# Optimization experiments

Measured on AMD Instinct MI355X. Metric: run time of the kernel, lower is better.

The kernel has to match this reference:

```python
import jax, jax.numpy as jnp
import numpy as np

N_T, D_MODEL, RANK, BATCH = 64, 1024, 8, 4096
THRESHOLD = 0.0  # jumprelu threshold (forward default)


def setup_inputs() -> dict:
    key = jax.random.key(0)
    k_x, k_v, k_u, k_e = jax.random.split(key, 4)
    scale = (1.0 / (D_MODEL * RANK)) ** 0.25
    x = jax.random.normal(k_x, (BATCH, D_MODEL), dtype=jnp.float32)
    V = jax.random.normal(k_v, (N_T, RANK, D_MODEL), dtype=jnp.float32) * scale
    U = jax.random.normal(k_u, (N_T, D_MODEL, RANK), dtype=jnp.float32) * scale
    encoder = jax.random.normal(k_e, (N_T, D_MODEL), dtype=jnp.float32)
    encoder = encoder / jnp.linalg.norm(encoder, axis=1, keepdims=True)
    bias = -jnp.ones((N_T,), dtype=jnp.float32)  # init_constant(bias, -1.0)
    return {"x": x, "V": V, "U": U, "encoder": encoder, "bias": bias}


def jumprelu(x, threshold=THRESHOLD):
    # forward: hard threshold x * 1[x > threshold]
    return x * (x > threshold).astype(x.dtype)


def reference(x, V, U, encoder, bias):
    # pre_acts: (batch, n)
    pre_acts = x @ encoder.T - bias
    gate = jumprelu(pre_acts)  # activation_fn='jumprelu', threshold=0.0
    # Vx: (n, batch, rank)
    Vx = jnp.einsum('nrd,bd->nbr', V, x)
    # UVx: (n, batch, d) -- the large intermediate a fused kernel would avoid
    UVx = jnp.einsum('ndr,nbr->nbd', U, Vx)
    # gated sum over transforms: (batch, d)
    output = jnp.einsum('nbd,bn->bd', UVx, gate)
    u_norms = jnp.linalg.norm(U.reshape(U.shape[0], -1), axis=1)
    v_norms = jnp.linalg.norm(V.reshape(V.shape[0], -1), axis=1)
    frobenius_norms = u_norms * v_norms / (D_MODEL * RANK) ** 0.5
    return output, gate, frobenius_norms
```

## Files before the change

kernel.cpp:

```cpp
#include <hip/hip_runtime.h>
#include <math.h>

#define BATCHN 4096
#define DMODEL 1024
#define NT 64
#define RANK 8
#define K2 512

typedef __attribute__((ext_vector_type(8))) short bf16x8;
typedef __attribute__((ext_vector_type(4))) float f32x4;

__device__ __forceinline__ void async16(void* lds, const void* g) {
    __builtin_amdgcn_global_load_lds(
        (const __attribute__((address_space(1))) void*)g,
        (__attribute__((address_space(3))) void*)lds, 16, 0, 0);
}

__device__ __forceinline__ short f2bf(float f) {
    unsigned u = __builtin_bit_cast(unsigned, f);
    u += 0x7fffu + ((u >> 16) & 1u);
    return (short)(u >> 16);
}

__device__ __forceinline__ bf16x8 cvt8(const float4 a, const float4 b) {
    bf16x8 o;
    o[0]=f2bf(a.x); o[1]=f2bf(a.y); o[2]=f2bf(a.z); o[3]=f2bf(a.w);
    o[4]=f2bf(b.x); o[5]=f2bf(b.y); o[6]=f2bf(b.z); o[7]=f2bf(b.w);
    return o;
}

__global__ __launch_bounds__(256) void gatevx_kernel(
    const float* __restrict__ x, const float* __restrict__ enc,
    const float* __restrict__ V, const float* __restrict__ U,
    const float* __restrict__ bias,
    float* __restrict__ gate_out, unsigned short* __restrict__ vx_out,
    unsigned short* __restrict__ Ub,
    float* __restrict__ su_part, float* __restrict__ sv_part)
{
    __shared__ unsigned short As[2][4096];
    __shared__ unsigned short Bs[2][4096];
    __shared__ float red[4];
    const int t = threadIdx.x;
    const int bn = blockIdx.x, bm = blockIdx.y;
    const int wave = t >> 6, lane = t & 63;

    if (bn == 9) {
        const int n = bm;
        const size_t base = (size_t)n * 8192;
        float s = 0.f;
        #pragma unroll
        for (int it = 0; it < 4; ++it) {
            const size_t e = base + it * 2048 + t * 8;
            float4 v0 = *(const float4*)(U + e);
            float4 v1 = *(const float4*)(U + e + 4);
            *(bf16x8*)(Ub + e) = cvt8(v0, v1);
            s += v0.x*v0.x + v0.y*v0.y + v0.z*v0.z + v0.w*v0.w
               + v1.x*v1.x + v1.y*v1.y + v1.z*v1.z + v1.w*v1.w;
        }
        #pragma unroll
        for (int off = 32; off; off >>= 1) s += __shfl_down(s, off);
        if ((t & 63) == 0) red[t >> 6] = s;
        __syncthreads();
        if (t == 0) su_part[n] = red[0] + red[1] + red[2] + red[3];
        return;
    }

    constexpr int BK = 64, KDIM = DMODEL, NIT = KDIM / BK;
    const int wm = wave & 1, wn = wave >> 1;
    const int lrow = lane >> 3, lchunk = lane & 7;
    const int l15 = lane & 15, lq = lane >> 4;

    f32x4 acc[2][2] = {};
    const size_t Arow0 = (size_t)bm * 64;
    const float* Bbase = (bn == 0) ? enc : V + (size_t)(bn - 1) * 64 * DMODEL;
    const bool doSV = (bn >= 1) && (bm == 0);
    float sv[2] = {0.f, 0.f};

    auto LOADAB = [&](int k0, float4* a, float4* b) {
        #pragma unroll
        for (int c = 0; c < 2; ++c) {
            const int row = (wave * 2 + c) * 8 + lrow;
            const int chunk = lchunk ^ lrow;
            const float* ax = x + (Arow0 + row) * DMODEL + k0 + chunk * 8;
            a[c*2]   = *(const float4*)ax;
            a[c*2+1] = *(const float4*)(ax + 4);
            const float* bx = Bbase + (size_t)row * DMODEL + k0 + chunk * 8;
            b[c*2]   = *(const float4*)bx;
            b[c*2+1] = *(const float4*)(bx + 4);
        }
    };
    auto WRITEAB = [&](int buf, const float4* a, const float4* b) {
        #pragma unroll
        for (int c = 0; c < 2; ++c) {
            *(bf16x8*)&As[buf][(wave * 2 + c) * 512 + lane * 8] = cvt8(a[c*2], a[c*2+1]);
            *(bf16x8*)&Bs[buf][(wave * 2 + c) * 512 + lane * 8] = cvt8(b[c*2], b[c*2+1]);
            if (doSV) {
                const float4 b0 = b[c*2], b1 = b[c*2+1];
                sv[c] += b0.x*b0.x + b0.y*b0.y + b0.z*b0.z + b0.w*b0.w
                       + b1.x*b1.x + b1.y*b1.y + b1.z*b1.z + b1.w*b1.w;
            }
        }
    };
    auto COMPUTE = [&](int buf) {
        #pragma unroll
        for (int s = 0; s < 2; ++s) {
            bf16x8 af[2], bfr[2];
            const int kc = s * 4 + lq;
            #pragma unroll
            for (int i = 0; i < 2; ++i) {
                const int m = wm * 32 + i * 16 + l15;
                af[i] = *(const bf16x8*)&As[buf][m * BK + ((kc ^ (m & 7)) * 8)];
            }
            #pragma unroll
            for (int j = 0; j < 2; ++j) {
                const int n = wn * 32 + j * 16 + l15;
                bfr[j] = *(const bf16x8*)&Bs[buf][n * BK + ((kc ^ (n & 7)) * 8)];
            }
            #pragma unroll
            for (int i = 0; i < 2; ++i)
                #pragma unroll
                for (int j = 0; j < 2; ++j)
                    acc[i][j] = __builtin_amdgcn_mfma_f32_16x16x32_bf16(
                        af[i], bfr[j], acc[i][j], 0, 0, 0);
        }
    };

    {
        float4 a[4], b[4];
        LOADAB(0, a, b);
        WRITEAB(0, a, b);
    }
    __syncthreads();
    int cur = 0;
    for (int kt = 0; kt < NIT - 1; ++kt) {
        float4 a[4], b[4];
        LOADAB((kt + 1) * BK, a, b);
        COMPUTE(cur);
        WRITEAB(cur ^ 1, a, b);
        __syncthreads();
        cur ^= 1;
    }
    COMPUTE(cur);

    if (doSV) {
        #pragma unroll
        for (int c = 0; c < 2; ++c) {
            float s = sv[c];
            #pragma unroll
            for (int off = 32; off; off >>= 1) s += __shfl_down(s, off);
            if (lane == 0) sv_part[(bn - 1) * 8 + wave * 2 + c] = s;
        }
    }
    __syncthreads();

    if (bn == 0) {
        float* Cs = (float*)&As[0][0];
        #pragma unroll
        for (int i = 0; i < 2; ++i) {
            const int rowb = wm * 32 + i * 16 + lq * 4;
            #pragma unroll
            for (int j = 0; j < 2; ++j) {
                const int col = wn * 32 + j * 16 + l15;
                const float bz = bias[col];
                #pragma unroll
                for (int r = 0; r < 4; ++r) {
                    const float p = acc[i][j][r] - bz;
                    Cs[(rowb + r) * 64 + col] = p > 0.f ? p : 0.f;
                }
            }
        }
        __syncthreads();
        #pragma unroll
        for (int p = 0; p < 4; ++p) {
            const int row = p * 16 + (t >> 4);
            const int col = (t & 15) * 4;
            *(f32x4*)&gate_out[(size_t)(bm * 64 + row) * NT + col] =
                *(const f32x4*)&Cs[row * 64 + col];
        }
    } else {
        unsigned short* Cs16 = &As[0][0];
        #pragma unroll
        for (int i = 0; i < 2; ++i) {
            const int rowb = wm * 32 + i * 16 + lq * 4;
            #pragma unroll
            for (int j = 0; j < 2; ++j) {
                const int col = wn * 32 + j * 16 + l15;
                #pragma unroll
                for (int r = 0; r < 4; ++r)
                    Cs16[(rowb + r) * 64 + col] = (unsigned short)f2bf(acc[i][j][r]);
            }
        }
        __syncthreads();
        #pragma unroll
        for (int p = 0; p < 2; ++p) {
            const int row = p * 32 + (t >> 3);
            const int chunk = t & 7;
            *(bf16x8*)&vx_out[(size_t)(bm * 64 + row) * K2 + (bn - 1) * 64 + chunk * 8] =
                *(const bf16x8*)&Cs16[row * 64 + chunk * 8];
        }
    }
}

__global__ __launch_bounds__(256) void out_kernel(
    const unsigned short* __restrict__ vx, const float* __restrict__ gate,
    const unsigned short* __restrict__ Ub, float* __restrict__ out,
    const float* __restrict__ su_part, const float* __restrict__ sv_part,
    float* __restrict__ fro)
{
    constexpr int BK = 64, KDIM = K2, NIT = KDIM / BK;
    __shared__ unsigned short As[2][4096];
    __shared__ unsigned short Bs[2][8192];
    const int t = threadIdx.x;
    const int wave = t >> 6, lane = t & 63;
    const int bm = blockIdx.y, bn = blockIdx.x;
    const int wm = wave & 1, wn = wave >> 1;
    const int lrow = lane >> 3, lchunk = lane & 7;
    const int l15 = lane & 15, lq = lane >> 4;

    f32x4 acc[2][4] = {};

    auto LOADA = [&](int k0, bf16x8* v, float* g) {
        #pragma unroll
        for (int c = 0; c < 2; ++c) {
            const int row = (wave * 2 + c) * 8 + lrow;
            const int grow = bm * 64 + row;
            const int chunk = lchunk ^ lrow;
            v[c] = *(const bf16x8*)(vx + (size_t)grow * K2 + k0 + chunk * 8);
            g[c] = gate[(size_t)grow * NT + (k0 >> 3) + chunk];
        }
    };
    auto WRITEA = [&](int buf, const bf16x8* v, const float* g) {
        #pragma unroll
        for (int c = 0; c < 2; ++c) {
            bf16x8 o;
            #pragma unroll
            for (int e = 0; e < 8; ++e) {
                const float f = __builtin_bit_cast(float,
                    ((unsigned)(unsigned short)v[c][e]) << 16);
                o[e] = (short)(__builtin_bit_cast(unsigned, f * g[c]) >> 16);
            }
            *(bf16x8*)&As[buf][(wave * 2 + c) * 512 + lane * 8] = o;
        }
    };
    auto STAGEB = [&](int buf, int k0) {
        #pragma unroll
        for (int c = 0; c < 4; ++c) {
            const int n_local = wave * 2 + (c >> 1);
            const int dblk = c & 1;
            const int n_glob = (k0 >> 3) + n_local;
            async16(&Bs[buf][(n_local * 2 + dblk) * 512],
                    Ub + (size_t)n_glob * (DMODEL * RANK)
                       + (size_t)(bn * 128 + dblk * 64 + lane) * RANK);
        }
    };
    auto COMPUTE = [&](int buf) {
        #pragma unroll
        for (int s = 0; s < 2; ++s) {
            bf16x8 af[2], bfr[4];
            const int kc = s * 4 + lq;
            #pragma unroll
            for (int i = 0; i < 2; ++i) {
                const int m = wm * 32 + i * 16 + l15;
                af[i] = *(const bf16x8*)&As[buf][m * BK + ((kc ^ (m & 7)) * 8)];
            }
            #pragma unroll
            for (int j = 0; j < 4; ++j) {
                const int cl = wn * 64 + j * 16 + l15;
                bfr[j] = *(const bf16x8*)&Bs[buf][((kc * 2 + (cl >> 6)) * 64 + (cl & 63)) * 8];
            }
            #pragma unroll
            for (int i = 0; i < 2; ++i)
                #pragma unroll
                for (int j = 0; j < 4; ++j)
                    acc[i][j] = __builtin_amdgcn_mfma_f32_16x16x32_bf16(
                        af[i], bfr[j], acc[i][j], 0, 0, 0);
        }
    };

    {
        bf16x8 v[2]; float g[2];
        LOADA(0, v, g);
        STAGEB(0, 0);
        WRITEA(0, v, g);
    }
    __syncthreads();
    int cur = 0;
    for (int kt = 0; kt < NIT - 1; ++kt) {
        bf16x8 v[2]; float g[2];
        LOADA((kt + 1) * BK, v, g);
        STAGEB(cur ^ 1, (kt + 1) * BK);
        COMPUTE(cur);
        WRITEA(cur ^ 1, v, g);
        __syncthreads();
        cur ^= 1;
    }
    COMPUTE(cur);
    __syncthreads();

    float* Cs = (float*)&Bs[0][0];
    #pragma unroll
    for (int i = 0; i < 2; ++i) {
        const int rowb = wm * 32 + i * 16 + lq * 4;
        #pragma unroll
        for (int j = 0; j < 4; ++j) {
            const int col = wn * 64 + j * 16 + l15;
            #pragma unroll
            for (int r = 0; r < 4; ++r)
                Cs[(rowb + r) * 128 + col] = acc[i][j][r];
        }
    }
    __syncthreads();
    #pragma unroll
    for (int p = 0; p < 8; ++p) {
        const int row = p * 8 + (t >> 5);
        const int col = (t & 31) * 4;
        *(f32x4*)&out[(size_t)(bm * 64 + row) * DMODEL + bn * 128 + col] =
            *(const f32x4*)&Cs[row * 128 + col];
    }

    if (bn == 0 && bm == 0 && t < NT) {
        fro[t] = sqrtf(su_part[t]) * sqrtf(sv_part[t]) / sqrtf((float)(DMODEL * RANK));
    }
}

extern "C" void kernel_launch(void* const* d_in, const int* in_sizes, int n_in,
                              void* d_out, int out_size, void* d_ws, size_t ws_size,
                              hipStream_t stream) {
    const float* x    = (const float*)d_in[0];
    const float* V    = (const float*)d_in[1];
    const float* U    = (const float*)d_in[2];
    const float* enc  = (const float*)d_in[3];
    const float* bias = (const float*)d_in[4];

    float* out  = (float*)d_out;
    float* gate = out + (size_t)BATCHN * DMODEL;
    float* fro  = gate + (size_t)BATCHN * NT;

    char* ws = (char*)d_ws;
    unsigned short* Ub = (unsigned short*)ws;
    unsigned short* vx = (unsigned short*)(ws + 1048576);
    float* su_part     = (float*)(ws + 5242880);
    float* sv_part     = (float*)(ws + 5244928);

    gatevx_kernel<<<dim3(10, 64), 256, 0, stream>>>(
        x, enc, V, U, bias, gate, vx, Ub, su_part, sv_part);
    out_kernel<<<dim3(8, 64), 256, 0, stream>>>(
        vx, gate, Ub, out, su_part, sv_part, fro);
}
```

Measured before the change: 111.2 us.

## Remap workgroups for XCD locality and deepen register prefetch pipeline

Both kernels now use a 1D grid and remap block IDs so that consecutive tiles sharing the same x or vx rows land on the same XCD (bid&7 selects the XCD), which is meant to improve L2 reuse across the 8 chiplets. The main loops are unrolled by two with two register staging sets, so global loads for tile k+2 are issued before computing tile k. This raises register pressure, and the later of the two barriers in each step now also covers the loop tail, so the separate barrier after the loop was removed.

Result: faster. 103.2 us (-7.2%).

```diff
diff --git a/kernel.cpp b/kernel.cpp
--- a/kernel.cpp
+++ b/kernel.cpp
@@ -41,11 +41,12 @@
     __shared__ unsigned short Bs[2][4096];
     __shared__ float red[4];
     const int t = threadIdx.x;
-    const int bn = blockIdx.x, bm = blockIdx.y;
+    const int bid = blockIdx.x;
+    const int wgid = (bid & 7) * 80 + (bid >> 3);
     const int wave = t >> 6, lane = t & 63;
 
-    if (bn == 9) {
-        const int n = bm;
+    if (wgid >= 576) {
+        const int n = wgid - 576;
         const size_t base = (size_t)n * 8192;
         float s = 0.f;
         #pragma unroll
@@ -66,6 +67,7 @@
     }
 
     constexpr int BK = 64, KDIM = DMODEL, NIT = KDIM / BK;
+    const int bm = wgid / 9, bn = wgid % 9;
     const int wm = wave & 1, wn = wave >> 1;
     const int lrow = lane >> 3, lchunk = lane & 7;
     const int l15 = lane & 15, lq = lane >> 4;
@@ -125,22 +127,21 @@
         }
     };
 
-    {
-        float4 a[4], b[4];
-        LOADAB(0, a, b);
-        WRITEAB(0, a, b);
-    }
+    float4 a0[4], b0[4], a1[4], b1[4];
+    LOADAB(0, a0, b0);
+    WRITEAB(0, a0, b0);
+    LOADAB(BK, a1, b1);
     __syncthreads();
-    int cur = 0;
-    for (int kt = 0; kt < NIT - 1; ++kt) {
-        float4 a[4], b[4];
-        LOADAB((kt + 1) * BK, a, b);
-        COMPUTE(cur);
-        WRITEAB(cur ^ 1, a, b);
-        __syncthreads();
-        cur ^= 1;
-    }
-    COMPUTE(cur);
+    for (int kt = 0; kt < NIT; kt += 2) {
+        if (kt + 2 < NIT) LOADAB((kt + 2) * BK, a0, b0);
+        COMPUTE(0);
+        WRITEAB(1, a1, b1);
+        __syncthreads();
+        if (kt + 3 < NIT) LOADAB((kt + 3) * BK, a1, b1);
+        COMPUTE(1);
+        if (kt + 2 < NIT) WRITEAB(0, a0, b0);
+        __syncthreads();
+    }
 
     if (doSV) {
         #pragma unroll
@@ -151,7 +152,6 @@
             if (lane == 0) sv_part[(bn - 1) * 8 + wave * 2 + c] = s;
         }
     }
-    __syncthreads();
 
     if (bn == 0) {
         float* Cs = (float*)&As[0][0];
@@ -211,8 +211,10 @@
     __shared__ unsigned short As[2][4096];
     __shared__ unsigned short Bs[2][8192];
     const int t = threadIdx.x;
+    const int bid = blockIdx.x;
+    const int wgid = (bid & 7) * 64 + (bid >> 3);
+    const int bm = wgid >> 3, bn = wgid & 7;
     const int wave = t >> 6, lane = t & 63;
-    const int bm = blockIdx.y, bn = blockIdx.x;
     const int wm = wave & 1, wn = wave >> 1;
     const int lrow = lane >> 3, lchunk = lane & 7;
     const int l15 = lane & 15, lq = lane >> 4;
@@ -277,25 +279,24 @@
         }
     };
 
-    {
-        bf16x8 v[2]; float g[2];
-        LOADA(0, v, g);
-        STAGEB(0, 0);
-        WRITEA(0, v, g);
-    }
+    bf16x8 v0[2], v1[2]; float g0[2], g1[2];
+    LOADA(0, v0, g0);
+    STAGEB(0, 0);
+    WRITEA(0, v0, g0);
+    LOADA(BK, v1, g1);
     __syncthreads();
-    int cur = 0;
-    for (int kt = 0; kt < NIT - 1; ++kt) {
-        bf16x8 v[2]; float g[2];
-        LOADA((kt + 1) * BK, v, g);
-        STAGEB(cur ^ 1, (kt + 1) * BK);
-        COMPUTE(cur);
-        WRITEA(cur ^ 1, v, g);
-        __syncthreads();
-        cur ^= 1;
-    }
-    COMPUTE(cur);
-    __syncthreads();
+    for (int kt = 0; kt < NIT; kt += 2) {
+        if (kt + 2 < NIT) LOADA((kt + 2) * BK, v0, g0);
+        STAGEB(1, (kt + 1) * BK);
+        COMPUTE(0);
+        WRITEA(1, v1, g1);
+        __syncthreads();
+        if (kt + 3 < NIT) LOADA((kt + 3) * BK, v1, g1);
+        if (kt + 2 < NIT) STAGEB(0, (kt + 2) * BK);
+        COMPUTE(1);
+        if (kt + 2 < NIT) WRITEA(0, v0, g0);
+        __syncthreads();
+    }
 
     float* Cs = (float*)&Bs[0][0];
     #pragma unroll
@@ -342,8 +343,8 @@
     float* su_part     = (float*)(ws + 5242880);
     float* sv_part     = (float*)(ws + 5244928);
 
-    gatevx_kernel<<<dim3(10, 64), 256, 0, stream>>>(
+    gatevx_kernel<<<640, 256, 0, stream>>>(
         x, enc, V, U, bias, gate, vx, Ub, su_part, sv_part);
-    out_kernel<<<dim3(8, 64), 256, 0, stream>>>(
+    out_kernel<<<512, 256, 0, stream>>>(
         vx, gate, Ub, out, su_part, sv_part, fro);
 }
```
